# Kernel tuning notes

Measured on AMD Instinct MI355X. Metric: run time of the kernel, lower is better.

## Reference

```python
import jax, jax.numpy as jnp
import numpy as np
import math

U_CONST = 0.5
FAC_DECAY = math.exp(-1.0 / 100.0)  # tau_fac = 100
DEP_DECAY = math.exp(-1.0 / 200.0)  # tau_dep = 200
BATCH, IN_F, OUT_F = 8192, 4096, 128


def setup_inputs() -> dict:
    key = jax.random.key(0)
    k1, k2 = jax.random.split(key)
    # binary spikes in {0,1} as float32
    pre_spike = jax.random.randint(k1, (BATCH, IN_F), 0, 2).astype(jnp.float32)
    # weight ~ U[0.25, 0.75) per torch.rand(out,in)*0.5 + 0.25
    weight = jax.random.uniform(k2, (OUT_F, IN_F), dtype=jnp.float32) * 0.5 + 0.25
    u = jnp.full((BATCH, IN_F), U_CONST, dtype=jnp.float32)  # facilitation state
    x = jnp.ones((BATCH, IN_F), dtype=jnp.float32)           # depression state
    return {"pre_spike": pre_spike, "weight": weight, "u": u, "x": x}


def reference(pre_spike, weight, u, x):
    # release probability per (batch, in_feature); fold onto pre_spike instead of
    # materializing the (batch, out, in) effective weight (same math).
    release_prob = u * x
    out = jnp.einsum('bi,oi->bo', pre_spike * release_prob, weight)  # [B, out]

    # STP state updates (facilitation then depression; x-update uses NEW u)
    u_fd = u * FAC_DECAY
    u_new = u_fd + U_CONST * (1.0 - u_fd) * pre_spike
    x_new = x * DEP_DECAY + (1.0 - x) * DEP_DECAY * (1.0 - pre_spike * u_new)
    return out, u_new, x_new
```

## Files before the change

### kernel.cpp

```cpp
#include <hip/hip_runtime.h>
#include <hip/hip_bf16.h>
#include <cstdint>

#define BATCH 8192
#define IN_F  4096
#define OUT_F 128
#define KSPLIT 8
#define KSLICE (IN_F / KSPLIT)
#define NKS    (KSLICE / 32)
#define FD 0.99004983374916811f
#define DD 0.99501247919268232f

typedef __attribute__((ext_vector_type(4))) float f32x4;
typedef __attribute__((ext_vector_type(8))) float f32x8;
typedef __attribute__((ext_vector_type(8))) short bf16x8;

__device__ __forceinline__ unsigned short f2bf(float f){
  union { float f; unsigned u; } v; v.f = f;
  unsigned u = v.u;
  return (unsigned short)((u + 0x7FFFu + ((u >> 16) & 1u)) >> 16);
}

__global__ __launch_bounds__(256) void prep_weight_kernel(const float* __restrict__ w,
                                                          unsigned short* __restrict__ wf){
  const int f  = blockIdx.x * 256 + threadIdx.x;
  const int l  = f & 63;
  const int ct = (f >> 6) & 7;
  const int ks = f >> 9;
  const int row = ct * 16 + (l & 15);
  const int k   = ks * 32 + ((l >> 4) << 3);
  const f32x4* src = reinterpret_cast<const f32x4*>(w + (size_t)row * IN_F + k);
  f32x4 a = src[0], b = src[1];
  union { bf16x8 v; unsigned short s[8]; } o;
  o.s[0]=f2bf(a[0]); o.s[1]=f2bf(a[1]); o.s[2]=f2bf(a[2]); o.s[3]=f2bf(a[3]);
  o.s[4]=f2bf(b[0]); o.s[5]=f2bf(b[1]); o.s[6]=f2bf(b[2]); o.s[7]=f2bf(b[3]);
  *reinterpret_cast<bf16x8*>(wf + (size_t)f * 8) = o.v;
}

__global__ __launch_bounds__(256, 3) void stp_fused7(
    const float* __restrict__ pre, const float* __restrict__ uin,
    const float* __restrict__ xin, const unsigned short* __restrict__ wf,
    float* __restrict__ out, float* __restrict__ un_out, float* __restrict__ xn_out)
{
  const int tid = threadIdx.x;
  const int wv  = tid >> 6;
  const int l   = tid & 63;

  const int kslice  = blockIdx.x & (KSPLIT - 1);
  const int rowBase = (blockIdx.x >> 3) * 64 + wv * 16;
  const size_t base = (size_t)(rowBase + (l & 15)) * IN_F + kslice * KSLICE + ((l >> 4) << 3);

  const bf16x8* wfp = reinterpret_cast<const bf16x8*>(wf);

  f32x4 acc[8];
  #pragma unroll
  for (int ct = 0; ct < 8; ++ct) acc[ct] = (f32x4){0.f,0.f,0.f,0.f};

  f32x8 s0 = *reinterpret_cast<const f32x8*>(pre + base);
  f32x8 u0 = *reinterpret_cast<const f32x8*>(uin + base);
  f32x8 x0 = *reinterpret_cast<const f32x8*>(xin + base);
  f32x8 s1 = *reinterpret_cast<const f32x8*>(pre + base + 32);
  f32x8 u1 = *reinterpret_cast<const f32x8*>(uin + base + 32);
  f32x8 x1 = *reinterpret_cast<const f32x8*>(xin + base + 32);

  #pragma unroll 2
  for (int ks = 0; ks < NKS; ++ks){
    const size_t g   = base + (size_t)(ks << 5);
    const int    gks = kslice * NKS + ks;

    bf16x8 b[8];
    #pragma unroll
    for (int ct = 0; ct < 8; ++ct)
      b[ct] = wfp[(size_t)((gks * 8 + ct) << 6) + l];

    f32x8 un, xn;
    union { bf16x8 v; unsigned short s[8]; } af;
    #pragma unroll
    for (int j = 0; j < 8; ++j){
      const float s = s0[j], u = u0[j], x = x0[j];
      af.s[j] = f2bf(u * x * s);
      const float ufd = u * FD;
      const float unj = ufd + 0.5f * (1.0f - ufd) * s;
      un[j] = unj;
      xn[j] = x * DD + (1.0f - x) * DD * (1.0f - s * unj);
    }

    *reinterpret_cast<f32x8*>(un_out + g) = un;
    *reinterpret_cast<f32x8*>(xn_out + g) = xn;

    f32x8 s2, u2, x2;
    if (ks + 2 < NKS){
      const size_t g2 = base + (size_t)((ks + 2) << 5);
      s2 = *reinterpret_cast<const f32x8*>(pre + g2);
      u2 = *reinterpret_cast<const f32x8*>(uin + g2);
      x2 = *reinterpret_cast<const f32x8*>(xin + g2);
    }

    #pragma unroll
    for (int ct = 0; ct < 8; ++ct)
      acc[ct] = __builtin_amdgcn_mfma_f32_16x16x32_bf16(af.v, b[ct], acc[ct], 0, 0, 0);

    s0 = s1; u0 = u1; x0 = x1;
    s1 = s2; u1 = u2; x1 = x2;
  }

  const int col0 = l & 15;
  const int r0   = rowBase + ((l >> 4) << 2);
  #pragma unroll
  for (int ct = 0; ct < 8; ++ct){
    #pragma unroll
    for (int rg = 0; rg < 4; ++rg){
      unsafeAtomicAdd(&out[(size_t)(r0 + rg) * OUT_F + ct * 16 + col0], acc[ct][rg]);
    }
  }
}

extern "C" void kernel_launch(void* const* d_in, const int* in_sizes, int n_in,
                              void* d_out, int out_size, void* d_ws, size_t ws_size,
                              hipStream_t stream){
  const float* pre = (const float*)d_in[0];
  const float* w   = (const float*)d_in[1];
  const float* u   = (const float*)d_in[2];
  const float* x   = (const float*)d_in[3];
  float* out    = (float*)d_out;
  float* un_out = out + (size_t)BATCH * OUT_F;
  float* xn_out = un_out + (size_t)BATCH * IN_F;
  unsigned short* wf = (unsigned short*)d_ws;

  hipMemsetAsync(out, 0, (size_t)BATCH * OUT_F * sizeof(float), stream);

  prep_weight_kernel<<<256, 256, 0, stream>>>(w, wf);
  stp_fused7<<<(BATCH / 64) * KSPLIT, 256, 0, stream>>>(pre, u, x, wf, out, un_out, xn_out);
}
```

Measured before the change: 179.7 us.

## Split fused STP kernel into elementwise pass and separate bf16 GEMM

```diff
diff --git a/kernel.cpp b/kernel.cpp
--- a/kernel.cpp
+++ b/kernel.cpp
@@ -5,6 +5,7 @@
 #define BATCH 8192
 #define IN_F  4096
 #define OUT_F 128
+#define N_ELEM ((size_t)BATCH * IN_F)
 #define KSPLIT 8
 #define KSLICE (IN_F / KSPLIT)
 #define NKS    (KSLICE / 32)
@@ -12,7 +13,6 @@
 #define DD 0.99501247919268232f
 
 typedef __attribute__((ext_vector_type(4))) float f32x4;
-typedef __attribute__((ext_vector_type(8))) float f32x8;
 typedef __attribute__((ext_vector_type(8))) short bf16x8;
 
 __device__ __forceinline__ unsigned short f2bf(float f){
@@ -37,10 +37,42 @@
   *reinterpret_cast<bf16x8*>(wf + (size_t)f * 8) = o.v;
 }
 
-__global__ __launch_bounds__(256, 3) void stp_fused7(
+__global__ __launch_bounds__(256) void stp_elem4(
     const float* __restrict__ pre, const float* __restrict__ uin,
-    const float* __restrict__ xin, const unsigned short* __restrict__ wf,
-    float* __restrict__ out, float* __restrict__ un_out, float* __restrict__ xn_out)
+    const float* __restrict__ xin,
+    float* __restrict__ un_out, float* __restrict__ xn_out,
+    unsigned short* __restrict__ r_out)
+{
+  const size_t nvec = N_ELEM / 4;
+  const size_t stride = (size_t)gridDim.x * 256;
+  for (size_t i = (size_t)blockIdx.x * 256 + threadIdx.x; i < nvec; i += stride){
+    const size_t e = i * 4;
+    f32x4 s4 = *reinterpret_cast<const f32x4*>(pre + e);
+    f32x4 u4 = *reinterpret_cast<const f32x4*>(uin + e);
+    f32x4 x4 = *reinterpret_cast<const f32x4*>(xin + e);
+    f32x4 un, xn;
+    unsigned short rb[4];
+    #pragma unroll
+    for (int j = 0; j < 4; ++j){
+      const float s = s4[j], u = u4[j], x = x4[j];
+      rb[j] = f2bf(u * x * s);
+      const float ufd = u * FD;
+      const float unj = ufd + 0.5f * (1.0f - ufd) * s;
+      un[j] = unj;
+      xn[j] = x * DD + (1.0f - x) * DD * (1.0f - s * unj);
+    }
+    *reinterpret_cast<f32x4*>(un_out + e) = un;
+    *reinterpret_cast<f32x4*>(xn_out + e) = xn;
+    uint2 pk;
+    pk.x = (unsigned)rb[0] | ((unsigned)rb[1] << 16);
+    pk.y = (unsigned)rb[2] | ((unsigned)rb[3] << 16);
+    *reinterpret_cast<uint2*>(r_out + e) = pk;
+  }
+}
+
+__global__ __launch_bounds__(256) void stp_gemm2(
+    const unsigned short* __restrict__ r, const unsigned short* __restrict__ wf,
+    float* __restrict__ out)
 {
   const int tid = threadIdx.x;
   const int wv  = tid >> 6;
@@ -56,52 +88,20 @@
   #pragma unroll
   for (int ct = 0; ct < 8; ++ct) acc[ct] = (f32x4){0.f,0.f,0.f,0.f};
 
-  f32x8 s0 = *reinterpret_cast<const f32x8*>(pre + base);
-  f32x8 u0 = *reinterpret_cast<const f32x8*>(uin + base);
-  f32x8 x0 = *reinterpret_cast<const f32x8*>(xin + base);
-  f32x8 s1 = *reinterpret_cast<const f32x8*>(pre + base + 32);
-  f32x8 u1 = *reinterpret_cast<const f32x8*>(uin + base + 32);
-  f32x8 x1 = *reinterpret_cast<const f32x8*>(xin + base + 32);
-
   #pragma unroll 2
   for (int ks = 0; ks < NKS; ++ks){
-    const size_t g   = base + (size_t)(ks << 5);
-    const int    gks = kslice * NKS + ks;
+    const int gks = kslice * NKS + ks;
+
+    bf16x8 af = *reinterpret_cast<const bf16x8*>(r + base + (ks << 5));
 
     bf16x8 b[8];
     #pragma unroll
     for (int ct = 0; ct < 8; ++ct)
       b[ct] = wfp[(size_t)((gks * 8 + ct) << 6) + l];
 
-    f32x8 un, xn;
-    union { bf16x8 v; unsigned short s[8]; } af;
-    #pragma unroll
-    for (int j = 0; j < 8; ++j){
-      const float s = s0[j], u = u0[j], x = x0[j];
-      af.s[j] = f2bf(u * x * s);
-      const float ufd = u * FD;
-      const float unj = ufd + 0.5f * (1.0f - ufd) * s;
-      un[j] = unj;
-      xn[j] = x * DD + (1.0f - x) * DD * (1.0f - s * unj);
-    }
-
-    *reinterpret_cast<f32x8*>(un_out + g) = un;
-    *reinterpret_cast<f32x8*>(xn_out + g) = xn;
-
-    f32x8 s2, u2, x2;
-    if (ks + 2 < NKS){
-      const size_t g2 = base + (size_t)((ks + 2) << 5);
-      s2 = *reinterpret_cast<const f32x8*>(pre + g2);
-      u2 = *reinterpret_cast<const f32x8*>(uin + g2);
-      x2 = *reinterpret_cast<const f32x8*>(xin + g2);
-    }
-
     #pragma unroll
     for (int ct = 0; ct < 8; ++ct)
-      acc[ct] = __builtin_amdgcn_mfma_f32_16x16x32_bf16(af.v, b[ct], acc[ct], 0, 0, 0);
-
-    s0 = s1; u0 = u1; x0 = x1;
-    s1 = s2; u1 = u2; x1 = x2;
+      acc[ct] = __builtin_amdgcn_mfma_f32_16x16x32_bf16(af, b[ct], acc[ct], 0, 0, 0);
   }
 
   const int col0 = l & 15;
@@ -124,11 +124,14 @@
   const float* x   = (const float*)d_in[3];
   float* out    = (float*)d_out;
   float* un_out = out + (size_t)BATCH * OUT_F;
-  float* xn_out = un_out + (size_t)BATCH * IN_F;
+  float* xn_out = un_out + N_ELEM;
+
   unsigned short* wf = (unsigned short*)d_ws;
+  unsigned short* r  = (unsigned short*)((char*)d_ws + (size_t)(1 << 20));
 
   hipMemsetAsync(out, 0, (size_t)BATCH * OUT_F * sizeof(float), stream);
 
   prep_weight_kernel<<<256, 256, 0, stream>>>(w, wf);
-  stp_fused7<<<(BATCH / 64) * KSPLIT, 256, 0, stream>>>(pre, u, x, wf, out, un_out, xn_out);
+  stp_elem4<<<2048, 256, 0, stream>>>(pre, u, x, un_out, xn_out, r);
+  stp_gemm2<<<(BATCH / 64) * KSPLIT, 256, 0, stream>>>(r, wf, out);
 }
```

Result: slower. 207.5 us (+15.4%).
